# Kernel optimization log

Measured on AMD Instinct MI355X. Metric: run time of the kernel, lower is better.

The kernel has to match this reference:

```python
import jax, jax.numpy as jnp
import numpy as np

H = 48; W = 48; WS = 8; NH = 12; FTH = 0.4; EPS = 1e-6


def _layernorm(x, w, b):
    mu = jnp.mean(x, axis=-1, keepdims=True)
    var = jnp.mean((x - mu) ** 2, axis=-1, keepdims=True)
    return (x - mu) * jax.lax.rsqrt(var + EPS) * w + b


def _mha(x, w_qkv, b_qkv, w_o, b_o, key_mask=None):
    # x: (Bn, N, C); w_qkv: (3, C, C); key_mask: (Bn, N) bool or None
    Bn, N, C = x.shape
    d = C // NH
    qkv = jnp.einsum('bnc,tcd->tbnd', x, w_qkv) + b_qkv[:, None, None, :]
    q, k, v = [t.reshape(Bn, N, NH, d).transpose(0, 2, 1, 3) for t in qkv]
    s = jnp.einsum('bhqd,bhkd->bhqk', q, k) / jnp.sqrt(jnp.asarray(d, x.dtype))
    if key_mask is not None:
        s = jnp.where(key_mask[:, None, None, :], s, jnp.asarray(-1e9, s.dtype))
    p = jax.nn.softmax(s, axis=-1)
    ctx = jnp.einsum('bhqk,bhkd->bhqd', p, v).transpose(0, 2, 1, 3).reshape(Bn, N, C)
    return ctx @ w_o + b_o


def _forward(x, mask, w_qkv_g, b_qkv_g, w_o_g, b_o_g, w_qkv_l, b_qkv_l, w_o_l, b_o_l,
             ln1_w, ln1_b, ln2_w, ln2_b, w_fc1, b_fc1, w_fc2, b_fc2):
    B, L, C = x.shape
    shortcut = x
    xn = _layernorm(x, ln1_w, ln1_b)

    # avg_pool2d(mask, 4, 4) -> (B, H, W); fg/bg split
    pooled = mask.reshape(B, 1, H, 4, W, 4).mean(axis=(3, 5))[:, 0]      # (B,H,W)
    fg = pooled > FTH                                                    # bool (B,H,W)
    fg_tok = fg.reshape(B, L)
    bg = (~fg).astype(x.dtype)
    # window-level bg mask: avg_pool(bg, WS) > 0 -> window contains any bg token
    bg_win = bg.reshape(B, H // WS, WS, W // WS, WS).mean(axis=(2, 4)) > 0.0   # (B, nH, nW)
    bg_win_tok = jnp.broadcast_to(bg_win[:, :, None, :, None],
                                  (B, H // WS, WS, W // WS, WS)).reshape(B, L)

    # local windowed attention on all windows (equivalent on bg windows; masked out elsewhere)
    xw = xn.reshape(B, H // WS, WS, W // WS, WS, C).transpose(0, 1, 3, 2, 4, 5)
    xw = xw.reshape(-1, WS * WS, C)                                      # (B*nWin, WS*WS, C)
    lout = _mha(xw, w_qkv_l, b_qkv_l, w_o_l, b_o_l)
    lout = lout.reshape(B, H // WS, W // WS, WS, WS, C).transpose(0, 1, 3, 2, 4, 5)
    lout = lout.reshape(B, L, C)

    # global attention with fg key mask (fg queries attend fg keys only)
    gout = _mha(xn, w_qkv_g, b_qkv_g, w_o_g, b_o_g, key_mask=fg_tok)

    # scatter-back semantics: fg positions take global output; bg-window positions take local output; rest zero
    zero = jnp.zeros((), x.dtype)
    x_new = jnp.where(fg_tok[..., None], gout,
                      jnp.where(bg_win_tok[..., None], lout, zero))

    x1 = shortcut + x_new
    h = _layernorm(x1, ln2_w, ln2_b)
    h = jax.nn.gelu(h @ w_fc1 + b_fc1, approximate=False) @ w_fc2 + b_fc2
    return x1 + h


def setup_inputs() -> dict:
    key = jax.random.key(0)
    ks = jax.random.split(key, 8)
    B, L, C, M = 2, H * W, 768, 3072
    s = 0.02
    return {
        'x': jax.random.normal(ks[0], (B, L, C), jnp.float32),
        'mask': jax.random.uniform(ks[1], (B, 1, 4 * H, 4 * W), jnp.float32),
        'w_qkv_g': jax.random.normal(ks[2], (3, C, C), jnp.float32) * s,
        'b_qkv_g': jnp.zeros((3, C), jnp.float32),
        'w_o_g': jax.random.normal(ks[3], (C, C), jnp.float32) * s,
        'b_o_g': jnp.zeros((C,), jnp.float32),
        'w_qkv_l': jax.random.normal(ks[4], (3, C, C), jnp.float32) * s,
        'b_qkv_l': jnp.zeros((3, C), jnp.float32),
        'w_o_l': jax.random.normal(ks[5], (C, C), jnp.float32) * s,
        'b_o_l': jnp.zeros((C,), jnp.float32),
        'ln1_w': jnp.ones((C,), jnp.float32),
        'ln1_b': jnp.zeros((C,), jnp.float32),
        'ln2_w': jnp.ones((C,), jnp.float32),
        'ln2_b': jnp.zeros((C,), jnp.float32),
        'w_fc1': jax.random.normal(ks[6], (C, M), jnp.float32) * s,
        'b_fc1': jnp.zeros((M,), jnp.float32),
        'w_fc2': jax.random.normal(ks[7], (M, C), jnp.float32) * s,
        'b_fc2': jnp.zeros((C,), jnp.float32),
    }


def reference(x, mask, w_qkv_g, b_qkv_g, w_o_g, b_o_g, w_qkv_l, b_qkv_l, w_o_l, b_o_l,
              ln1_w, ln1_b, ln2_w, ln2_b, w_fc1, b_fc1, w_fc2, b_fc2):
    return _forward(x, mask, w_qkv_g, b_qkv_g, w_o_g, b_o_g, w_qkv_l, b_qkv_l, w_o_l, b_o_l,
                    ln1_w, ln1_b, ln2_w, ln2_b, w_fc1, b_fc1, w_fc2, b_fc2)
```

## Files before the change

kernel.cpp:

```cpp
#include <hip/hip_runtime.h>
#include <math.h>

#define Lh 2304
#define Ch 768
#define NHh 12
#define Bh 2
#define QS2 3072

typedef unsigned short ushort_t;
typedef unsigned int uint_t;
typedef __attribute__((ext_vector_type(8))) short bf16x8;
typedef __attribute__((ext_vector_type(4))) float f32x4;
#define MFMA16(a, b, c) __builtin_amdgcn_mfma_f32_16x16x32_bf16(a, b, c, 0, 0, 0)

#define SCL2 0.18033688f
#define MSK2 1.4426950e9f
#if __has_builtin(__builtin_amdgcn_exp2f)
#define EXP2F(x) __builtin_amdgcn_exp2f(x)
#else
#define EXP2F(x) exp2f(x)
#endif

__device__ __forceinline__ ushort_t f2bf(float f) {
    union { float f; uint_t u; } v; v.f = f;
    uint_t u = v.u + 0x7fffu + ((v.u >> 16) & 1u);
    return (ushort_t)(u >> 16);
}
__device__ __forceinline__ uint_t pack2bf(float a, float b) {
    return (uint_t)f2bf(a) | ((uint_t)f2bf(b) << 16);
}

__device__ __forceinline__ void llds16(ushort_t* dst, const ushort_t* src) {
    __builtin_amdgcn_global_load_lds(
        (__attribute__((address_space(1))) void*)(const_cast<ushort_t*>(src)),
        (__attribute__((address_space(3))) void*)dst, 16, 0, 0);
}

__device__ __forceinline__ void ln_body(const float* __restrict__ x, const float* __restrict__ w,
                                        const float* __restrict__ b, ushort_t* __restrict__ y,
                                        int row, float* red)
{
    int tid = threadIdx.x;
    const float* xr = x + (size_t)row * Ch;
    float v0 = xr[tid], v1 = xr[tid + 256], v2 = xr[tid + 512];
    red[tid] = v0 + v1 + v2;
    __syncthreads();
    for (int st = 128; st > 0; st >>= 1) {
        if (tid < st) red[tid] += red[tid + st];
        __syncthreads();
    }
    float mean = red[0] * (1.0f / 768.0f);
    __syncthreads();
    float d0 = v0 - mean, d1 = v1 - mean, d2 = v2 - mean;
    red[tid] = d0 * d0 + d1 * d1 + d2 * d2;
    __syncthreads();
    for (int st = 128; st > 0; st >>= 1) {
        if (tid < st) red[tid] += red[tid + st];
        __syncthreads();
    }
    float rstd = rsqrtf(red[0] * (1.0f / 768.0f) + 1e-6f);
    ushort_t* yr = y + (size_t)row * Ch;
    yr[tid]       = f2bf(d0 * rstd * w[tid]       + b[tid]);
    yr[tid + 256] = f2bf(d1 * rstd * w[tid + 256] + b[tid + 256]);
    yr[tid + 512] = f2bf(d2 * rstd * w[tid + 512] + b[tid + 512]);
}

__global__ __launch_bounds__(256)
void layernorm_bf16_kernel(const float* __restrict__ x, const float* __restrict__ w,
                           const float* __restrict__ b, ushort_t* __restrict__ y)
{
    __shared__ float red[256];
    ln_body(x, w, b, y, blockIdx.x, red);
}

__global__ __launch_bounds__(256)
void ln_mask_kernel(const float* __restrict__ x, const float* __restrict__ w,
                    const float* __restrict__ b, ushort_t* __restrict__ y,
                    const float* __restrict__ mask, float* __restrict__ fg,
                    float* __restrict__ bgw)
{
    __shared__ float red[256];
    int bid = blockIdx.x;
    if (bid < 4608) {
        ln_body(x, w, b, y, bid, red);
        return;
    }
    int win = bid - 4608;
    int tid = threadIdx.x;
    if (tid >= 64) return;
    int bb = win / 36, ww = win % 36;
    int wi = ww / 6, wj = ww % 6;
    int i = wi * 8 + (tid >> 3), j = wj * 8 + (tid & 7);
    const float* mb = mask + (size_t)bb * 192 * 192 + (size_t)(i * 4) * 192 + j * 4;
    float s = 0.0f;
    #pragma unroll
    for (int di = 0; di < 4; ++di) {
        float4 v = *(const float4*)(mb + (size_t)di * 192);
        s += v.x + v.y + v.z + v.w;
    }
    float f = (s * (1.0f / 16.0f) > 0.4f) ? 1.0f : 0.0f;
    fg[bb * Lh + i * 48 + j] = f;
    unsigned long long bg = __ballot(f == 0.0f);
    if (tid == 0) bgw[win] = bg ? 1.0f : 0.0f;
}

__global__ __launch_bounds__(256)
void transpose_all_kernel(const float* __restrict__ w_qkv_g, const float* __restrict__ w_qkv_l,
                          const float* __restrict__ w_o_g, const float* __restrict__ w_o_l,
                          const float* __restrict__ w_fc1, const float* __restrict__ w_fc2,
                          const float* __restrict__ b_qkv_g, const float* __restrict__ b_qkv_l,
                          ushort_t* __restrict__ wtq, ushort_t* __restrict__ wt_o_g,
                          ushort_t* __restrict__ wt_o_l, ushort_t* __restrict__ wt_fc1,
                          ushort_t* __restrict__ wt_fc2, float* __restrict__ biasq)
{
    int blk = blockIdx.x;
    int tid = threadIdx.x;
    if (blk >= 2304) {
        int which = blk - 2304;
        const float* src = which ? b_qkv_l : b_qkv_g;
        float* dst = biasq + which * 2304;
        for (int i = tid; i < 2304; i += 256) dst[i] = src[i];
        return;
    }
    const float* W; ushort_t* D; int K, N, nx, bx;
    const size_t CC = (size_t)Ch * Ch;
    if (blk < 432)       { int t = blk / 144; bx = blk % 144;
                           W = w_qkv_g + t * CC; D = wtq + t * CC; K = 768; N = 768; nx = 12; }
    else if (blk < 864)  { int r = blk - 432; int t = r / 144; bx = r % 144;
                           W = w_qkv_l + t * CC; D = wtq + (size_t)2304 * 768 + t * CC;
                           K = 768; N = 768; nx = 12; }
    else if (blk < 1008) { bx = blk - 864;  W = w_o_g; D = wt_o_g; K = 768; N = 768; nx = 12; }
    else if (blk < 1152) { bx = blk - 1008; W = w_o_l; D = wt_o_l; K = 768; N = 768; nx = 12; }
    else if (blk < 1728) { bx = blk - 1152; W = w_fc1; D = wt_fc1; K = 768; N = 3072; nx = 48; }
    else                 { bx = blk - 1728; W = w_fc2; D = wt_fc2; K = 3072; N = 768; nx = 12; }
    int n0 = (bx % nx) * 64;
    int k0 = (bx / nx) * 64;
    __shared__ float T[64][65];
    #pragma unroll
    for (int i = 0; i < 4; ++i) {
        int lin = i * 256 + tid;
        int r = lin >> 4, c = (lin & 15) * 4;
        float4 v = *(const float4*)&W[(size_t)(k0 + r) * N + n0 + c];
        T[r][c] = v.x; T[r][c + 1] = v.y; T[r][c + 2] = v.z; T[r][c + 3] = v.w;
    }
    __syncthreads();
    #pragma unroll
    for (int i = 0; i < 4; ++i) {
        int lin = i * 256 + tid;
        int r = lin >> 4, c0 = (lin & 15) * 4;
        uint_t lo = pack2bf(T[c0][r], T[c0 + 1][r]);
        uint_t hi = pack2bf(T[c0 + 2][r], T[c0 + 3][r]);
        *(uint2*)&D[(size_t)(n0 + r) * K + k0 + c0] = make_uint2(lo, hi);
    }
}

template<int BNt, int VMODE>
__device__ __forceinline__ void gemm_body(
    const ushort_t* __restrict__ A, const ushort_t* __restrict__ Bt,
    const float* __restrict__ bias, const float* __restrict__ residual,
    void* __restrict__ C, ushort_t* __restrict__ vt,
    int M, int N, int K, int flags, int bm, int bn, ushort_t* pool)
{
    ushort_t (*AsL)[128 * 32] = (ushort_t(*)[128 * 32])pool;
    ushort_t (*BsL)[BNt * 32] = (ushort_t(*)[BNt * 32])(pool + 2 * 128 * 32);
    int tid = threadIdx.x;
    int lane = tid & 63;
    int wave = tid >> 6;
    int wm = wave >> 1, wn = wave & 1;
    int quad = lane >> 4, l15 = lane & 15;
    constexpr int NJ = BNt / 32;

    int srow = lane >> 2;
    int sg8 = ((lane & 3) ^ ((lane >> 3) & 3)) * 8;
    int fsw = (l15 >> 1) & 3;

    f32x4 acc[4][NJ];
    #pragma unroll
    for (int i = 0; i < 4; ++i)
        #pragma unroll
        for (int j = 0; j < NJ; ++j)
            acc[i][j] = (f32x4){0.f, 0.f, 0.f, 0.f};

    int iters = K / 32;
    llds16(&AsL[0][wave * 512], A + (size_t)(bm + wave * 16 + srow) * K + sg8);
    llds16(&AsL[0][(wave + 4) * 512], A + (size_t)(bm + (wave + 4) * 16 + srow) * K + sg8);
    llds16(&BsL[0][wave * 512], Bt + (size_t)(bn + wave * 16 + srow) * K + sg8);
    if (BNt == 128)
        llds16(&BsL[0][(wave + 4) * 512], Bt + (size_t)(bn + (wave + 4) * 16 + srow) * K + sg8);

    for (int kt = 0; kt < iters; ++kt) {
        int cur = kt & 1;
        __syncthreads();

        bf16x8 af[4], bfr[NJ];
        #pragma unroll
        for (int i = 0; i < 4; ++i)
            af[i] = *(const bf16x8*)&AsL[cur][(wm * 64 + i * 16 + l15) * 32 + ((quad ^ fsw) * 8)];
        #pragma unroll
        for (int j = 0; j < NJ; ++j)
            bfr[j] = *(const bf16x8*)&BsL[cur][(wn * (BNt / 2) + j * 16 + l15) * 32 + ((quad ^ fsw) * 8)];

        if (kt + 1 < iters) {
            int k0 = (kt + 1) * 32;
            int nxt = 1 - cur;
            llds16(&AsL[nxt][wave * 512], A + (size_t)(bm + wave * 16 + srow) * K + k0 + sg8);
            llds16(&AsL[nxt][(wave + 4) * 512], A + (size_t)(bm + (wave + 4) * 16 + srow) * K + k0 + sg8);
            llds16(&BsL[nxt][wave * 512], Bt + (size_t)(bn + wave * 16 + srow) * K + k0 + sg8);
            if (BNt == 128)
                llds16(&BsL[nxt][(wave + 4) * 512], Bt + (size_t)(bn + (wave + 4) * 16 + srow) * K + k0 + sg8);
        }

        if constexpr (VMODE == 0) {
            #pragma unroll
            for (int i = 0; i < 4; ++i)
                #pragma unroll
                for (int j = 0; j < NJ; ++j)
                    acc[i][j] = MFMA16(bfr[j], af[i], acc[i][j]);
        } else {
            #pragma unroll
            for (int i = 0; i < 4; ++i)
                #pragma unroll
                for (int j = 0; j < NJ; ++j)
                    acc[i][j] = MFMA16(af[i], bfr[j], acc[i][j]);
        }
    }

    if constexpr (VMODE == 1) {
        #pragma unroll
        for (int j = 0; j < NJ; ++j) {
            int col = bn + wn * (BNt / 2) + j * 16 + l15;
            int colp = col - ((col >= 3840) ? 3072 : 1536);
            float bc = bias[col];
            #pragma unroll
            for (int i = 0; i < 4; ++i) {
                int row0 = bm + wm * 64 + i * 16 + quad * 4;
                *(uint2*)&vt[(size_t)colp * 4608 + row0] =
                    make_uint2(pack2bf(acc[i][j][0] + bc, acc[i][j][1] + bc),
                               pack2bf(acc[i][j][2] + bc, acc[i][j][3] + bc));
            }
        }
        return;
    }

    #pragma unroll
    for (int i = 0; i < 4; ++i) {
        int row = bm + wm * 64 + i * 16 + l15;
        #pragma unroll
        for (int j = 0; j < NJ; ++j) {
            int col = bn + wn * (BNt / 2) + j * 16 + quad * 4;
            float4 bia = *(const float4*)&bias[col];
            float o0 = acc[i][j][0] + bia.x;
            float o1 = acc[i][j][1] + bia.y;
            float o2 = acc[i][j][2] + bia.z;
            float o3 = acc[i][j][3] + bia.w;
            if (flags & 1) {
                o0 = o0 * 0.5f * (1.0f + erff(o0 * 0.70710678f));
                o1 = o1 * 0.5f * (1.0f + erff(o1 * 0.70710678f));
                o2 = o2 * 0.5f * (1.0f + erff(o2 * 0.70710678f));
                o3 = o3 * 0.5f * (1.0f + erff(o3 * 0.70710678f));
            }
            if (residual) {
                float4 rs = *(const float4*)&residual[(size_t)row * N + col];
                o0 += rs.x; o1 += rs.y; o2 += rs.z; o3 += rs.w;
            }
            if (flags & 4) {
                int cq = col - ((col >= 2304) ? 768 : 0);
                *(uint2*)&((ushort_t*)C)[(size_t)row * QS2 + cq] =
                    make_uint2(pack2bf(o0, o1), pack2bf(o2, o3));
            } else if (flags & 2) {
                *(uint2*)&((ushort_t*)C)[(size_t)row * N + col] =
                    make_uint2(pack2bf(o0, o1), pack2bf(o2, o3));
            } else {
                *(float4*)&((float*)C)[(size_t)row * N + col] =
                    make_float4(o0, o1, o2, o3);
            }
        }
    }
}

template<int BNt>
__global__ __launch_bounds__(256)
void gemm_bf16_t(const ushort_t* __restrict__ A, const ushort_t* __restrict__ Bt,
                 const float* __restrict__ bias, const float* __restrict__ residual,
                 void* __restrict__ C, int M, int N, int K, int flags)
{
    __shared__ ushort_t pool[2 * 128 * 32 + 2 * BNt * 32];
    gemm_body<BNt, 0>(A, Bt, bias, residual, C, nullptr, M, N, K, flags,
                      blockIdx.y * 128, blockIdx.x * BNt, pool);
}

__global__ __launch_bounds__(256)
void qkv_gemm_kernel(const ushort_t* __restrict__ A, const ushort_t* __restrict__ Bt,
                     const float* __restrict__ biasq, ushort_t* __restrict__ qkv,
                     ushort_t* __restrict__ vt)
{
    __shared__ ushort_t pool[4 * 128 * 32];
    int bx = blockIdx.x;
    int bm = blockIdx.y * 128;
    if (bx < 24) {
        int bn = (bx < 12) ? bx * 128 : 2304 + (bx - 12) * 128;
        gemm_body<128, 0>(A, Bt, biasq, nullptr, qkv, nullptr, 4608, 4608, Ch, 4, bm, bn, pool);
    } else {
        int bxx = bx - 24;
        int bn = (bxx < 6) ? 1536 + bxx * 128 : 3840 + (bxx - 6) * 128;
        gemm_body<128, 1>(A, Bt, biasq, nullptr, nullptr, vt, 4608, 4608, Ch, 4, bm, bn, pool);
    }
}

__global__ __launch_bounds__(256)
void oproj_dual_kernel(const ushort_t* __restrict__ ctxg, const ushort_t* __restrict__ ctxl,
                       const ushort_t* __restrict__ Wg, const ushort_t* __restrict__ Wl,
                       const float* __restrict__ biasg, const float* __restrict__ biasl,
                       const float* __restrict__ x, float* __restrict__ x1,
                       const float* __restrict__ fg, const float* __restrict__ bgw)
{
    __shared__ ushort_t AgL[2][128 * 32];
    __shared__ ushort_t AlL[2][128 * 32];
    __shared__ ushort_t BgL[2][64 * 32];
    __shared__ ushort_t BlL[2][64 * 32];
    int bm = blockIdx.y * 128;
    int bn = blockIdx.x * 64;
    int tid = threadIdx.x;
    int lane = tid & 63;
    int wave = tid >> 6;
    int wm = wave >> 1, wn = wave & 1;
    int quad = lane >> 4, l15 = lane & 15;

    int srow = lane >> 2;
    int sg8 = ((lane & 3) ^ ((lane >> 3) & 3)) * 8;
    int fsw = (l15 >> 1) & 3;
    const int K = Ch, N = Ch, iters = Ch / 32;

    f32x4 accg[4][2], accl[4][2];
    #pragma unroll
    for (int i = 0; i < 4; ++i)
        #pragma unroll
        for (int j = 0; j < 2; ++j) {
            accg[i][j] = (f32x4){0.f, 0.f, 0.f, 0.f};
            accl[i][j] = (f32x4){0.f, 0.f, 0.f, 0.f};
        }

    llds16(&AgL[0][wave * 512], ctxg + (size_t)(bm + wave * 16 + srow) * K + sg8);
    llds16(&AgL[0][(wave + 4) * 512], ctxg + (size_t)(bm + (wave + 4) * 16 + srow) * K + sg8);
    llds16(&AlL[0][wave * 512], ctxl + (size_t)(bm + wave * 16 + srow) * K + sg8);
    llds16(&AlL[0][(wave + 4) * 512], ctxl + (size_t)(bm + (wave + 4) * 16 + srow) * K + sg8);
    llds16(&BgL[0][wave * 512], Wg + (size_t)(bn + wave * 16 + srow) * K + sg8);
    llds16(&BlL[0][wave * 512], Wl + (size_t)(bn + wave * 16 + srow) * K + sg8);

    for (int kt = 0; kt < iters; ++kt) {
        int cur = kt & 1;
        __syncthreads();
        bf16x8 afg[4], afl[4], bfg[2], bfl[2];
        #pragma unroll
        for (int i = 0; i < 4; ++i) {
            afg[i] = *(const bf16x8*)&AgL[cur][(wm * 64 + i * 16 + l15) * 32 + ((quad ^ fsw) * 8)];
            afl[i] = *(const bf16x8*)&AlL[cur][(wm * 64 + i * 16 + l15) * 32 + ((quad ^ fsw) * 8)];
        }
        #pragma unroll
        for (int j = 0; j < 2; ++j) {
            bfg[j] = *(const bf16x8*)&BgL[cur][(wn * 32 + j * 16 + l15) * 32 + ((quad ^ fsw) * 8)];
            bfl[j] = *(const bf16x8*)&BlL[cur][(wn * 32 + j * 16 + l15) * 32 + ((quad ^ fsw) * 8)];
        }
        if (kt + 1 < iters) {
            int k0 = (kt + 1) * 32;
            int nxt = 1 - cur;
            llds16(&AgL[nxt][wave * 512], ctxg + (size_t)(bm + wave * 16 + srow) * K + k0 + sg8);
            llds16(&AgL[nxt][(wave + 4) * 512], ctxg + (size_t)(bm + (wave + 4) * 16 + srow) * K + k0 + sg8);
            llds16(&AlL[nxt][wave * 512], ctxl + (size_t)(bm + wave * 16 + srow) * K + k0 + sg8);
            llds16(&AlL[nxt][(wave + 4) * 512], ctxl + (size_t)(bm + (wave + 4) * 16 + srow) * K + k0 + sg8);
            llds16(&BgL[nxt][wave * 512], Wg + (size_t)(bn + wave * 16 + srow) * K + k0 + sg8);
            llds16(&BlL[nxt][wave * 512], Wl + (size_t)(bn + wave * 16 + srow) * K + k0 + sg8);
        }
        #pragma unroll
        for (int i = 0; i < 4; ++i)
            #pragma unroll
            for (int j = 0; j < 2; ++j)
                accg[i][j] = MFMA16(bfg[j], afg[i], accg[i][j]);
        #pragma unroll
        for (int i = 0; i < 4; ++i)
            #pragma unroll
            for (int j = 0; j < 2; ++j)
                accl[i][j] = MFMA16(bfl[j], afl[i], accl[i][j]);
    }

    #pragma unroll
    for (int i = 0; i < 4; ++i) {
        int row = bm + wm * 64 + i * 16 + l15;
        int bb = (row >= Lh) ? 1 : 0;
        int n = row - bb * Lh;
        int ii = n / 48, jj = n % 48;
        float keepg = (fg[row] != 0.0f) ? 1.0f : 0.0f;
        float keepl = (keepg == 0.0f &&
                       bgw[bb * 36 + (ii >> 3) * 6 + (jj >> 3)] != 0.0f) ? 1.0f : 0.0f;
        #pragma unroll
        for (int j = 0; j < 2; ++j) {
            int col = bn + wn * 32 + j * 16 + quad * 4;
            float4 bg4 = *(const float4*)&biasg[col];
            float4 bl4 = *(const float4*)&biasl[col];
            float4 x4 = *(const float4*)&x[(size_t)row * N + col];
            float4 o;
            o.x = x4.x + keepg * (accg[i][j][0] + bg4.x) + keepl * (accl[i][j][0] + bl4.x);
            o.y = x4.y + keepg * (accg[i][j][1] + bg4.y) + keepl * (accl[i][j][1] + bl4.y);
            o.z = x4.z + keepg * (accg[i][j][2] + bg4.z) + keepl * (accl[i][j][2] + bl4.z);
            o.w = x4.w + keepg * (accg[i][j][3] + bg4.w) + keepl * (accl[i][j][3] + bl4.w);
            *(float4*)&x1[(size_t)row * N + col] = o;
        }
    }
}

__device__ __forceinline__ void attn_global_body(
    const ushort_t* __restrict__ QKV, const ushort_t* __restrict__ VT,
    const float* __restrict__ fg,
    float* __restrict__ Opart, float* __restrict__ Lpart,
    int tile, int h, int b, int half,
    ushort_t (*Ks)[2][64][32], ushort_t (*Vs)[2][64][32],
    ushort_t (*Ps)[72], float (*fgs)[64])
{
    int tid = threadIdx.x;
    int lane = tid & 63;
    int wave = tid >> 6;
    int quad = lane >> 4, l15 = lane & 15;
    int kb0 = half * 1152;

    bf16x8 aq[2][2];
    #pragma unroll
    for (int s = 0; s < 2; ++s) {
        int tok = tile * 128 + wave * 32 + s * 16 + l15;
        const ushort_t* qbase = QKV + (size_t)(b * Lh + tok) * QS2 + h * 64;
        #pragma unroll
        for (int step = 0; step < 2; ++step)
            aq[s][step] = *(const bf16x8*)(qbase + step * 32 + quad * 8);
    }

    int srow = lane >> 2;
    int sc = lane & 3;
    int krow = wave * 16 + srow;
    int scx = (sc ^ ((krow >> 1) & 3)) * 8;
    const ushort_t* ksrc = QKV + (size_t)(b * Lh + kb0 + krow) * QS2 + 768 + h * 64 + scx;
    const ushort_t* vsrc = VT + (size_t)(h * 64 + krow) * 4608 + b * Lh + kb0 + scx;

    float l_part[2] = {0.f, 0.f};
    f32x4 o_acc[2][4];
    #pragma unroll
    for (int s = 0; s < 2; ++s)
        #pragma unroll
        for (int t4 = 0; t4 < 4; ++t4) o_acc[s][t4] = (f32x4){0.f, 0.f, 0.f, 0.f};

    llds16(&Ks[0][0][wave * 16][0], ksrc);
    llds16(&Ks[0][1][wave * 16][0], ksrc + 32);
    llds16(&Vs[0][0][wave * 16][0], vsrc);
    llds16(&Vs[0][1][wave * 16][0], vsrc + 32);
    if (tid < 64) fgs[0][tid] = (fg[b * Lh + kb0 + tid] - 1.0f) * MSK2;

    int rfs = (l15 >> 1) & 3;

    for (int kt = 0; kt < 18; ++kt) {
        int cur = kt & 1, nxt = cur ^ 1;
        __syncthreads();

        bf16x8 bk[2][4];
        #pragma unroll
        for (int step = 0; step < 2; ++step)
            #pragma unroll
            for (int j4 = 0; j4 < 4; ++j4)
                bk[step][j4] = *(const bf16x8*)&Ks[cur][step][j4 * 16 + l15][(quad ^ rfs) * 8];

        if (kt + 1 < 18) {
            const ushort_t* kp = ksrc + (size_t)(kt + 1) * 64 * QS2;
            const ushort_t* vp = vsrc + (kt + 1) * 64;
            llds16(&Ks[nxt][0][wave * 16][0], kp);
            llds16(&Ks[nxt][1][wave * 16][0], kp + 32);
            llds16(&Vs[nxt][0][wave * 16][0], vp);
            llds16(&Vs[nxt][1][wave * 16][0], vp + 32);
            if (tid < 64) fgs[nxt][tid] = (fg[b * Lh + kb0 + (kt + 1) * 64 + tid] - 1.0f) * MSK2;
        }

        f32x4 s4[2][4];
        #pragma unroll
        for (int s = 0; s < 2; ++s)
            #pragma unroll
            for (int j4 = 0; j4 < 4; ++j4) s4[s][j4] = (f32x4){0.f, 0.f, 0.f, 0.f};
        #pragma unroll
        for (int step = 0; step < 2; ++step)
            #pragma unroll
            for (int s = 0; s < 2; ++s)
                #pragma unroll
                for (int j4 = 0; j4 < 4; ++j4)
                    s4[s][j4] = MFMA16(bk[step][j4], aq[s][step], s4[s][j4]);

        #pragma unroll
        for (int s = 0; s < 2; ++s) {
            int p0 = wave * 32 + s * 16;
            #pragma unroll
            for (int j4 = 0; j4 < 4; ++j4) {
                float4 mb4 = *(const float4*)&fgs[cur][j4 * 16 + quad * 4];
                float e0 = EXP2F(s4[s][j4][0] * SCL2 + mb4.x);
                float e1 = EXP2F(s4[s][j4][1] * SCL2 + mb4.y);
                float e2 = EXP2F(s4[s][j4][2] * SCL2 + mb4.z);
                float e3 = EXP2F(s4[s][j4][3] * SCL2 + mb4.w);
                l_part[s] += (e0 + e1) + (e2 + e3);
                uint_t a01 = __builtin_amdgcn_perm(__float_as_uint(e1), __float_as_uint(e0), 0x07060302u);
                uint_t a23 = __builtin_amdgcn_perm(__float_as_uint(e3), __float_as_uint(e2), 0x07060302u);
                *(uint2*)&Ps[p0 + l15][j4 * 16 + quad * 4] = make_uint2(a01, a23);
            }
        }
        #pragma unroll
        for (int step = 0; step < 2; ++step) {
            bf16x8 bv[4];
            #pragma unroll
            for (int t4 = 0; t4 < 4; ++t4)
                bv[t4] = *(const bf16x8*)&Vs[cur][step][t4 * 16 + l15][(quad ^ rfs) * 8];
            #pragma unroll
            for (int s = 0; s < 2; ++s) {
                int p0 = wave * 32 + s * 16;
                bf16x8 a = *(const bf16x8*)&Ps[p0 + l15][step * 32 + quad * 8];
                #pragma unroll
                for (int t4 = 0; t4 < 4; ++t4)
                    o_acc[s][t4] = MFMA16(bv[t4], a, o_acc[s][t4]);
            }
        }
    }

    #pragma unroll
    for (int s = 0; s < 2; ++s) {
        float v = l_part[s];
        v += __shfl_xor(v, 16, 64);
        v += __shfl_xor(v, 32, 64);
        int ql = wave * 32 + s * 16 + l15;
        int tok = tile * 128 + ql;
        float* op = Opart + ((size_t)half * 4608 + b * Lh + tok) * Ch + h * 64;
        #pragma unroll
        for (int t4 = 0; t4 < 4; ++t4)
            *(f32x4*)&op[t4 * 16 + quad * 4] = o_acc[s][t4];
        if (quad == 0)
            Lpart[((size_t)half * 4608 + b * Lh + tok) * NHh + h] = v;
    }
}

__device__ __forceinline__ void attn_local_body(
    const ushort_t* __restrict__ QKV, const ushort_t* __restrict__ VT,
    ushort_t* __restrict__ O, int tile, int h, int b,
    ushort_t (*Ks)[2][64][32], ushort_t (*Vs)[2][64][32], ushort_t (*Ps)[72])
{
    int tid = threadIdx.x;
    int lane = tid & 63;
    int wave = tid >> 6;
    int quad = lane >> 4, l15 = lane & 15;
    int wi = tile / 6, wj = tile % 6;

    bf16x8 aq[2];
    {
        int ql = wave * 16 + l15;
        int tok = (wi * 8 + (ql >> 3)) * 48 + wj * 8 + (ql & 7);
        const ushort_t* qbase = QKV + (size_t)(b * Lh + tok) * QS2 + 1536 + h * 64;
        #pragma unroll
        for (int step = 0; step < 2; ++step)
            aq[step] = *(const bf16x8*)(qbase + step * 32 + quad * 8);
    }

    {
        int srow = lane >> 2;
        int sc = lane & 3;
        int krow = wave * 16 + srow;
        int kfs = (krow >> 1) & 3;
        int tokK = (wi * 8 + (krow >> 3)) * 48 + wj * 8 + (krow & 7);
        const ushort_t* ksrc = QKV + (size_t)(b * Lh + tokK) * QS2 + 2304 + h * 64 + (sc ^ kfs) * 8;
        int c0 = sc ^ kfs;
        const ushort_t* vbase = VT + (size_t)(768 + h * 64 + krow) * 4608 + b * Lh + wj * 8;
        llds16(&Ks[0][0][wave * 16][0], ksrc);
        llds16(&Ks[0][1][wave * 16][0], ksrc + 32);
        llds16(&Vs[0][0][wave * 16][0], vbase + (wi * 8 + c0) * 48);
        llds16(&Vs[0][1][wave * 16][0], vbase + (wi * 8 + 4 + c0) * 48);
    }
    __syncthreads();

    float l_part = 0.f;
    f32x4 o_acc[4];
    #pragma unroll
    for (int t4 = 0; t4 < 4; ++t4) o_acc[t4] = (f32x4){0.f, 0.f, 0.f, 0.f};

    int rfs = (l15 >> 1) & 3;
    f32x4 s4[4];
    #pragma unroll
    for (int j4 = 0; j4 < 4; ++j4) s4[j4] = (f32x4){0.f, 0.f, 0.f, 0.f};
    #pragma unroll
    for (int step = 0; step < 2; ++step) {
        bf16x8 bk[4];
        #pragma unroll
        for (int j4 = 0; j4 < 4; ++j4)
            bk[j4] = *(const bf16x8*)&Ks[0][step][j4 * 16 + l15][(quad ^ rfs) * 8];
        #pragma unroll
        for (int j4 = 0; j4 < 4; ++j4)
            s4[j4] = MFMA16(bk[j4], aq[step], s4[j4]);
    }
    int p0 = wave * 16;
    #pragma unroll
    for (int j4 = 0; j4 < 4; ++j4) {
        float e0 = EXP2F(s4[j4][0] * SCL2);
        float e1 = EXP2F(s4[j4][1] * SCL2);
        float e2 = EXP2F(s4[j4][2] * SCL2);
        float e3 = EXP2F(s4[j4][3] * SCL2);
        l_part += (e0 + e1) + (e2 + e3);
        uint_t a01 = __builtin_amdgcn_perm(__float_as_uint(e1), __float_as_uint(e0), 0x07060302u);
        uint_t a23 = __builtin_amdgcn_perm(__float_as_uint(e3), __float_as_uint(e2), 0x07060302u);
        *(uint2*)&Ps[p0 + l15][j4 * 16 + quad * 4] = make_uint2(a01, a23);
    }
    #pragma unroll
    for (int step = 0; step < 2; ++step) {
        bf16x8 bv[4];
        #pragma unroll
        for (int t4 = 0; t4 < 4; ++t4)
            bv[t4] = *(const bf16x8*)&Vs[0][step][t4 * 16 + l15][(quad ^ rfs) * 8];
        bf16x8 a = *(const bf16x8*)&Ps[p0 + l15][step * 32 + quad * 8];
        #pragma unroll
        for (int t4 = 0; t4 < 4; ++t4)
            o_acc[t4] = MFMA16(bv[t4], a, o_acc[t4]);
    }

    {
        float v = l_part;
        v += __shfl_xor(v, 16, 64);
        v += __shfl_xor(v, 32, 64);
        float inv = 1.0f / v;
        int ql = wave * 16 + l15;
        int tok = (wi * 8 + (ql >> 3)) * 48 + wj * 8 + (ql & 7);
        ushort_t* ob = O + (size_t)(b * Lh + tok) * Ch + h * 64;
        #pragma unroll
        for (int t4 = 0; t4 < 4; ++t4) {
            *(uint2*)&ob[t4 * 16 + quad * 4] =
                make_uint2(pack2bf(o_acc[t4][0] * inv, o_acc[t4][1] * inv),
                           pack2bf(o_acc[t4][2] * inv, o_acc[t4][3] * inv));
        }
    }
}

__global__ __launch_bounds__(256)
void attn_fused_kernel(const ushort_t* __restrict__ QKV, const ushort_t* __restrict__ VT,
                       const float* __restrict__ fg,
                       float* __restrict__ Opart, float* __restrict__ Lpart,
                       ushort_t* __restrict__ ctxl)
{
    __shared__ __align__(16) ushort_t Ks[2][2][64][32];
    __shared__ __align__(16) ushort_t Vs[2][2][64][32];
    __shared__ __align__(16) ushort_t Ps[128][72];
    __shared__ float fgs[2][64];

    int bid = blockIdx.x;
    if (bid < 864) {
        int gid = (bid & 7) * 108 + (bid >> 3);
        int half = gid / 432;
        int rem = gid % 432;
        int tile = rem % 18;
        int h = (rem / 18) % NHh;
        int b = rem / 216;
        attn_global_body(QKV, VT, fg, Opart, Lpart, tile, h, b, half, Ks, Vs, Ps, fgs);
    } else {
        int rr = bid - 864;
        int lid = (rr & 7) * 108 + (rr >> 3);
        int tile = lid % 36;
        int h = (lid / 36) % NHh;
        int b = lid / 432;
        attn_local_body(QKV, VT, ctxl, tile, h, b, Ks, Vs, Ps);
    }
}

__global__ __launch_bounds__(192)
void attn_merge_kernel(const float* __restrict__ Op, const float* __restrict__ Lp,
                       ushort_t* __restrict__ ctxg)
{
    int r = blockIdx.x;
    int tid = threadIdx.x;
    int d = tid * 4;
    int h = d >> 6;
    float la = Lp[(size_t)r * NHh + h];
    float lb = Lp[((size_t)4608 + r) * NHh + h];
    float inv = 1.0f / (la + lb);
    const float* pa = Op + (size_t)r * Ch + d;
    const float* pb = Op + (size_t)4608 * Ch + (size_t)r * Ch + d;
    float4 a = *(const float4*)pa;
    float4 b4 = *(const float4*)pb;
    *(uint2*)&ctxg[(size_t)r * Ch + d] =
        make_uint2(pack2bf((a.x + b4.x) * inv, (a.y + b4.y) * inv),
                   pack2bf((a.z + b4.z) * inv, (a.w + b4.w) * inv));
}

extern "C" void kernel_launch(void* const* d_in, const int* in_sizes, int n_in,
                              void* d_out, int out_size, void* d_ws, size_t ws_size,
                              hipStream_t stream)
{
    const float* x       = (const float*)d_in[0];
    const float* mask    = (const float*)d_in[1];
    const float* w_qkv_g = (const float*)d_in[2];
    const float* b_qkv_g = (const float*)d_in[3];
    const float* w_o_g   = (const float*)d_in[4];
    const float* b_o_g   = (const float*)d_in[5];
    const float* w_qkv_l = (const float*)d_in[6];
    const float* b_qkv_l = (const float*)d_in[7];
    const float* w_o_l   = (const float*)d_in[8];
    const float* b_o_l   = (const float*)d_in[9];
    const float* ln1_w   = (const float*)d_in[10];
    const float* ln1_b   = (const float*)d_in[11];
    const float* ln2_w   = (const float*)d_in[12];
    const float* ln2_b   = (const float*)d_in[13];
    const float* w_fc1   = (const float*)d_in[14];
    const float* b_fc1   = (const float*)d_in[15];
    const float* w_fc2   = (const float*)d_in[16];
    const float* b_fc2   = (const float*)d_in[17];
    float* out = (float*)d_out;

    const size_t U = (size_t)Bh * Lh * Ch;
    char* p = (char*)d_ws;
    ushort_t* qkvb = (ushort_t*)p;        p += (size_t)4608 * 3072 * 2;
    ushort_t* vtb  = (ushort_t*)p;        p += (size_t)1536 * 4608 * 2;
    ushort_t* midb = qkvb;
    ushort_t* ctxg = (ushort_t*)p;        p += U * 2;
    ushort_t* ctxl = (ushort_t*)p;        p += U * 2;
    ushort_t* xnb  = (ushort_t*)p;        p += U * 2;
    float*    Opart = (float*)p;          p += (size_t)2 * U * 4;
    float*    Lpart = (float*)p;          p += (size_t)2 * 4608 * NHh * 4;
    float*    x1   = Opart;
    ushort_t* wtq  = (ushort_t*)p;        p += (size_t)4608 * 768 * 2;
    ushort_t* wt_o_g = (ushort_t*)p;      p += (size_t)768 * 768 * 2;
    ushort_t* wt_o_l = (ushort_t*)p;      p += (size_t)768 * 768 * 2;
    ushort_t* wt_fc1 = (ushort_t*)p;      p += (size_t)3072 * 768 * 2;
    ushort_t* wt_fc2 = (ushort_t*)p;      p += (size_t)768 * 3072 * 2;
    float*    biasq  = (float*)p;         p += 4608 * 4;
    float*    fg     = (float*)p;         p += Bh * Lh * 4;
    float*    bgw    = (float*)p;

    const int Mrows = Bh * Lh;
    dim3 blk(256);

    transpose_all_kernel<<<2306, blk, 0, stream>>>(
        w_qkv_g, w_qkv_l, w_o_g, w_o_l, w_fc1, w_fc2, b_qkv_g, b_qkv_l,
        wtq, wt_o_g, wt_o_l, wt_fc1, wt_fc2, biasq);

    ln_mask_kernel<<<4680, blk, 0, stream>>>(x, ln1_w, ln1_b, xnb, mask, fg, bgw);

    qkv_gemm_kernel<<<dim3(36, Mrows / 128), blk, 0, stream>>>(
        xnb, wtq, biasq, qkvb, vtb);

    attn_fused_kernel<<<1728, blk, 0, stream>>>(qkvb, vtb, fg, Opart, Lpart, ctxl);
    attn_merge_kernel<<<Mrows, dim3(192), 0, stream>>>(Opart, Lpart, ctxg);

    oproj_dual_kernel<<<dim3(Ch / 64, Mrows / 128), blk, 0, stream>>>(
        ctxg, ctxl, wt_o_g, wt_o_l, b_o_g, b_o_l, x, x1, fg, bgw);

    layernorm_bf16_kernel<<<Mrows, blk, 0, stream>>>(x1, ln2_w, ln2_b, xnb);

    gemm_bf16_t<128><<<dim3(3072 / 128, Mrows / 128), blk, 0, stream>>>(
        xnb, wt_fc1, b_fc1, nullptr, midb, Mrows, 3072, Ch, 1 | 2);
    gemm_bf16_t<64><<<dim3(Ch / 64, Mrows / 128), blk, 0, stream>>>(
        midb, wt_fc2, b_fc2, x1, out, Mrows, Ch, 3072, 0);
}
```

Before: 397.2 us.

## Split-K the FC2 GEMM into two halves and move LDS fragment reads after prefetch

The FC2 GEMM (K=3072) is split along K into two z-slices that write fp32 partials into a reused workspace. A new merge kernel sums the partials and adds bias and the residual. This doubles the block count from 216 to 432 to fill more compute units. Separately, the GEMM, o-proj and attention loops now issue the next tile's global-to-LDS loads before reading the current fragments from LDS. The cost is extra fp32 partial traffic and one more kernel launch.

```diff
diff --git a/kernel.cpp b/kernel.cpp
--- a/kernel.cpp
+++ b/kernel.cpp
@@ -159,7 +159,7 @@
     const ushort_t* __restrict__ A, const ushort_t* __restrict__ Bt,
     const float* __restrict__ bias, const float* __restrict__ residual,
     void* __restrict__ C, ushort_t* __restrict__ vt,
-    int M, int N, int K, int flags, int bm, int bn, ushort_t* pool)
+    int M, int N, int K, int ld, int flags, int bm, int bn, ushort_t* pool)
 {
     ushort_t (*AsL)[128 * 32] = (ushort_t(*)[128 * 32])pool;
     ushort_t (*BsL)[BNt * 32] = (ushort_t(*)[BNt * 32])(pool + 2 * 128 * 32);
@@ -182,33 +182,33 @@
             acc[i][j] = (f32x4){0.f, 0.f, 0.f, 0.f};
 
     int iters = K / 32;
-    llds16(&AsL[0][wave * 512], A + (size_t)(bm + wave * 16 + srow) * K + sg8);
-    llds16(&AsL[0][(wave + 4) * 512], A + (size_t)(bm + (wave + 4) * 16 + srow) * K + sg8);
-    llds16(&BsL[0][wave * 512], Bt + (size_t)(bn + wave * 16 + srow) * K + sg8);
+    llds16(&AsL[0][wave * 512], A + (size_t)(bm + wave * 16 + srow) * ld + sg8);
+    llds16(&AsL[0][(wave + 4) * 512], A + (size_t)(bm + (wave + 4) * 16 + srow) * ld + sg8);
+    llds16(&BsL[0][wave * 512], Bt + (size_t)(bn + wave * 16 + srow) * ld + sg8);
     if (BNt == 128)
-        llds16(&BsL[0][(wave + 4) * 512], Bt + (size_t)(bn + (wave + 4) * 16 + srow) * K + sg8);
+        llds16(&BsL[0][(wave + 4) * 512], Bt + (size_t)(bn + (wave + 4) * 16 + srow) * ld + sg8);
 
     for (int kt = 0; kt < iters; ++kt) {
         int cur = kt & 1;
         __syncthreads();
 
-        bf16x8 af[4], bfr[NJ];
-        #pragma unroll
-        for (int i = 0; i < 4; ++i)
-            af[i] = *(const bf16x8*)&AsL[cur][(wm * 64 + i * 16 + l15) * 32 + ((quad ^ fsw) * 8)];
-        #pragma unroll
-        for (int j = 0; j < NJ; ++j)
-            bfr[j] = *(const bf16x8*)&BsL[cur][(wn * (BNt / 2) + j * 16 + l15) * 32 + ((quad ^ fsw) * 8)];
-
         if (kt + 1 < iters) {
             int k0 = (kt + 1) * 32;
             int nxt = 1 - cur;
-            llds16(&AsL[nxt][wave * 512], A + (size_t)(bm + wave * 16 + srow) * K + k0 + sg8);
-            llds16(&AsL[nxt][(wave + 4) * 512], A + (size_t)(bm + (wave + 4) * 16 + srow) * K + k0 + sg8);
-            llds16(&BsL[nxt][wave * 512], Bt + (size_t)(bn + wave * 16 + srow) * K + k0 + sg8);
+            llds16(&AsL[nxt][wave * 512], A + (size_t)(bm + wave * 16 + srow) * ld + k0 + sg8);
+            llds16(&AsL[nxt][(wave + 4) * 512], A + (size_t)(bm + (wave + 4) * 16 + srow) * ld + k0 + sg8);
+            llds16(&BsL[nxt][wave * 512], Bt + (size_t)(bn + wave * 16 + srow) * ld + k0 + sg8);
             if (BNt == 128)
-                llds16(&BsL[nxt][(wave + 4) * 512], Bt + (size_t)(bn + (wave + 4) * 16 + srow) * K + k0 + sg8);
-        }
+                llds16(&BsL[nxt][(wave + 4) * 512], Bt + (size_t)(bn + (wave + 4) * 16 + srow) * ld + k0 + sg8);
+        }
+
+        bf16x8 af[4], bfr[NJ];
+        #pragma unroll
+        for (int i = 0; i < 4; ++i)
+            af[i] = *(const bf16x8*)&AsL[cur][(wm * 64 + i * 16 + l15) * 32 + ((quad ^ fsw) * 8)];
+        #pragma unroll
+        for (int j = 0; j < NJ; ++j)
+            bfr[j] = *(const bf16x8*)&BsL[cur][(wn * (BNt / 2) + j * 16 + l15) * 32 + ((quad ^ fsw) * 8)];
 
         if constexpr (VMODE == 0) {
             #pragma unroll
@@ -248,11 +248,14 @@
         #pragma unroll
         for (int j = 0; j < NJ; ++j) {
             int col = bn + wn * (BNt / 2) + j * 16 + quad * 4;
-            float4 bia = *(const float4*)&bias[col];
-            float o0 = acc[i][j][0] + bia.x;
-            float o1 = acc[i][j][1] + bia.y;
-            float o2 = acc[i][j][2] + bia.z;
-            float o3 = acc[i][j][3] + bia.w;
+            float o0 = acc[i][j][0];
+            float o1 = acc[i][j][1];
+            float o2 = acc[i][j][2];
+            float o3 = acc[i][j][3];
+            if (!(flags & 8)) {
+                float4 bia = *(const float4*)&bias[col];
+                o0 += bia.x; o1 += bia.y; o2 += bia.z; o3 += bia.w;
+            }
             if (flags & 1) {
                 o0 = o0 * 0.5f * (1.0f + erff(o0 * 0.70710678f));
                 o1 = o1 * 0.5f * (1.0f + erff(o1 * 0.70710678f));
@@ -282,10 +285,14 @@
 __global__ __launch_bounds__(256)
 void gemm_bf16_t(const ushort_t* __restrict__ A, const ushort_t* __restrict__ Bt,
                  const float* __restrict__ bias, const float* __restrict__ residual,
-                 void* __restrict__ C, int M, int N, int K, int flags)
+                 void* __restrict__ C, int M, int N, int K, int ld, int flags)
 {
     __shared__ ushort_t pool[2 * 128 * 32 + 2 * BNt * 32];
-    gemm_body<BNt, 0>(A, Bt, bias, residual, C, nullptr, M, N, K, flags,
+    int kz = blockIdx.z;
+    const ushort_t* Az = A + (size_t)kz * K;
+    const ushort_t* Btz = Bt + (size_t)kz * K;
+    void* Cz = (char*)C + (size_t)kz * M * N * sizeof(float) * ((flags & 8) ? 1 : 0);
+    gemm_body<BNt, 0>(Az, Btz, bias, residual, Cz, nullptr, M, N, K, ld, flags,
                       blockIdx.y * 128, blockIdx.x * BNt, pool);
 }
 
@@ -299,12 +306,27 @@
     int bm = blockIdx.y * 128;
     if (bx < 24) {
         int bn = (bx < 12) ? bx * 128 : 2304 + (bx - 12) * 128;
-        gemm_body<128, 0>(A, Bt, biasq, nullptr, qkv, nullptr, 4608, 4608, Ch, 4, bm, bn, pool);
+        gemm_body<128, 0>(A, Bt, biasq, nullptr, qkv, nullptr, 4608, 4608, Ch, Ch, 4, bm, bn, pool);
     } else {
         int bxx = bx - 24;
         int bn = (bxx < 6) ? 1536 + bxx * 128 : 3840 + (bxx - 6) * 128;
-        gemm_body<128, 1>(A, Bt, biasq, nullptr, nullptr, vt, 4608, 4608, Ch, 4, bm, bn, pool);
-    }
+        gemm_body<128, 1>(A, Bt, biasq, nullptr, nullptr, vt, 4608, 4608, Ch, Ch, 4, bm, bn, pool);
+    }
+}
+
+__global__ __launch_bounds__(192)
+void fc2_merge_kernel(const float* __restrict__ Fp, const float* __restrict__ x1,
+                      const float* __restrict__ bias, float* __restrict__ out)
+{
+    int r = blockIdx.x;
+    int d = threadIdx.x * 4;
+    float4 a = *(const float4*)&Fp[(size_t)r * Ch + d];
+    float4 b = *(const float4*)&Fp[(size_t)(4608 + r) * Ch + d];
+    float4 xr = *(const float4*)&x1[(size_t)r * Ch + d];
+    float4 bi = *(const float4*)&bias[d];
+    *(float4*)&out[(size_t)r * Ch + d] =
+        make_float4(xr.x + bi.x + a.x + b.x, xr.y + bi.y + a.y + b.y,
+                    xr.z + bi.z + a.z + b.z, xr.w + bi.w + a.w + b.w);
 }
 
 __global__ __launch_bounds__(256)
@@ -350,17 +372,7 @@
     for (int kt = 0; kt < iters; ++kt) {
         int cur = kt & 1;
         __syncthreads();
-        bf16x8 afg[4], afl[4], bfg[2], bfl[2];
-        #pragma unroll
-        for (int i = 0; i < 4; ++i) {
-            afg[i] = *(const bf16x8*)&AgL[cur][(wm * 64 + i * 16 + l15) * 32 + ((quad ^ fsw) * 8)];
-            afl[i] = *(const bf16x8*)&AlL[cur][(wm * 64 + i * 16 + l15) * 32 + ((quad ^ fsw) * 8)];
-        }
-        #pragma unroll
-        for (int j = 0; j < 2; ++j) {
-            bfg[j] = *(const bf16x8*)&BgL[cur][(wn * 32 + j * 16 + l15) * 32 + ((quad ^ fsw) * 8)];
-            bfl[j] = *(const bf16x8*)&BlL[cur][(wn * 32 + j * 16 + l15) * 32 + ((quad ^ fsw) * 8)];
-        }
+
         if (kt + 1 < iters) {
             int k0 = (kt + 1) * 32;
             int nxt = 1 - cur;
@@ -370,6 +382,18 @@
             llds16(&AlL[nxt][(wave + 4) * 512], ctxl + (size_t)(bm + (wave + 4) * 16 + srow) * K + k0 + sg8);
             llds16(&BgL[nxt][wave * 512], Wg + (size_t)(bn + wave * 16 + srow) * K + k0 + sg8);
             llds16(&BlL[nxt][wave * 512], Wl + (size_t)(bn + wave * 16 + srow) * K + k0 + sg8);
+        }
+
+        bf16x8 afg[4], afl[4], bfg[2], bfl[2];
+        #pragma unroll
+        for (int i = 0; i < 4; ++i) {
+            afg[i] = *(const bf16x8*)&AgL[cur][(wm * 64 + i * 16 + l15) * 32 + ((quad ^ fsw) * 8)];
+            afl[i] = *(const bf16x8*)&AlL[cur][(wm * 64 + i * 16 + l15) * 32 + ((quad ^ fsw) * 8)];
+        }
+        #pragma unroll
+        for (int j = 0; j < 2; ++j) {
+            bfg[j] = *(const bf16x8*)&BgL[cur][(wn * 32 + j * 16 + l15) * 32 + ((quad ^ fsw) * 8)];
+            bfl[j] = *(const bf16x8*)&BlL[cur][(wn * 32 + j * 16 + l15) * 32 + ((quad ^ fsw) * 8)];
         }
         #pragma unroll
         for (int i = 0; i < 4; ++i)
@@ -458,13 +482,6 @@
         int cur = kt & 1, nxt = cur ^ 1;
         __syncthreads();
 
-        bf16x8 bk[2][4];
-        #pragma unroll
-        for (int step = 0; step < 2; ++step)
-            #pragma unroll
-            for (int j4 = 0; j4 < 4; ++j4)
-                bk[step][j4] = *(const bf16x8*)&Ks[cur][step][j4 * 16 + l15][(quad ^ rfs) * 8];
-
         if (kt + 1 < 18) {
             const ushort_t* kp = ksrc + (size_t)(kt + 1) * 64 * QS2;
             const ushort_t* vp = vsrc + (kt + 1) * 64;
@@ -474,6 +491,13 @@
             llds16(&Vs[nxt][1][wave * 16][0], vp + 32);
             if (tid < 64) fgs[nxt][tid] = (fg[b * Lh + kb0 + (kt + 1) * 64 + tid] - 1.0f) * MSK2;
         }
+
+        bf16x8 bk[2][4];
+        #pragma unroll
+        for (int step = 0; step < 2; ++step)
+            #pragma unroll
+            for (int j4 = 0; j4 < 4; ++j4)
+                bk[step][j4] = *(const bf16x8*)&Ks[cur][step][j4 * 16 + l15][(quad ^ rfs) * 8];
 
         f32x4 s4[2][4];
         #pragma unroll
@@ -713,6 +737,7 @@
     ushort_t* qkvb = (ushort_t*)p;        p += (size_t)4608 * 3072 * 2;
     ushort_t* vtb  = (ushort_t*)p;        p += (size_t)1536 * 4608 * 2;
     ushort_t* midb = qkvb;
+    float*    Fpart = (float*)vtb;
     ushort_t* ctxg = (ushort_t*)p;        p += U * 2;
     ushort_t* ctxl = (ushort_t*)p;        p += U * 2;
     ushort_t* xnb  = (ushort_t*)p;        p += U * 2;
@@ -749,7 +774,8 @@
     layernorm_bf16_kernel<<<Mrows, blk, 0, stream>>>(x1, ln2_w, ln2_b, xnb);
 
     gemm_bf16_t<128><<<dim3(3072 / 128, Mrows / 128), blk, 0, stream>>>(
-        xnb, wt_fc1, b_fc1, nullptr, midb, Mrows, 3072, Ch, 1 | 2);
-    gemm_bf16_t<64><<<dim3(Ch / 64, Mrows / 128), blk, 0, stream>>>(
-        midb, wt_fc2, b_fc2, x1, out, Mrows, Ch, 3072, 0);
-}
+        xnb, wt_fc1, b_fc1, nullptr, midb, Mrows, 3072, Ch, Ch, 1 | 2);
+    gemm_bf16_t<64><<<dim3(Ch / 64, Mrows / 128, 2), blk, 0, stream>>>(
+        midb, wt_fc2, b_fc2, nullptr, Fpart, Mrows, Ch, 1536, 3072, 8);
+    fc2_merge_kernel<<<Mrows, dim3(192), 0, stream>>>(Fpart, x1, b_fc2, out);
+}
```

Measured after the change: 414.2 us. 4.3% more time.
